# Kernel tuning notes

Measured on AMD Instinct MI355X. Metric: run time of the kernel, lower is better.

Reference implementation:

```python
import jax, jax.numpy as jnp
import numpy as np

EMBED = 1024
HEADS = 16
HEAD_DIM = EMBED // HEADS
MAX_SEQ = 5000
THETA = 10000.0
BATCH = 16
SEQ_K = 1024
SEQ_Q = 512


def _rope_tables():
    inv = 1.0 / (THETA ** (np.arange(0, EMBED, 2)[: EMBED // 2] / EMBED))
    ang = np.outer(np.arange(MAX_SEQ), inv)  # [MAX_SEQ, EMBED//2]
    return jnp.asarray(np.cos(ang), jnp.float32), jnp.asarray(np.sin(ang), jnp.float32)

COS_T, SIN_T = _rope_tables()


def _apply_rope(x, idx):
    # x: [B, S, E]; idx: [B, S]; pairs are (x[...,2i], x[...,2i+1]) across the FULL embed dim
    B, S, E = x.shape
    xp = x.reshape(B, S, E // 2, 2)
    xr, xi = xp[..., 0], xp[..., 1]
    c, s = COS_T[idx], SIN_T[idx]  # [B, S, E//2]
    return jnp.stack([xr * c - xi * s, xr * s + xi * c], axis=-1).reshape(B, S, E)


def _attn_mask(key_padding_mask):
    # (causal triu OR key padding) AND NOT eye  (eye keeps diagonal attendable), then cut query rows
    tri = jnp.triu(jnp.ones((SEQ_K, SEQ_K), bool), k=1)
    m = jnp.logical_or(tri[None], key_padding_mask[:, None, :])  # [B, K, K]
    m = jnp.logical_and(m, ~jnp.eye(SEQ_K, dtype=bool)[None])
    return m[:, -SEQ_Q:, :]  # [B, Q, K]


def setup_inputs() -> dict:
    key = jax.random.key(0)
    ks = jax.random.split(key, 16)
    def lin(i):
        W = jax.random.normal(ks[i], (EMBED, EMBED), jnp.float32) / np.sqrt(EMBED).astype(np.float32)
        b = jnp.zeros((EMBED,), jnp.float32)
        return W, b
    Wq, bq = lin(0); Wk, bk = lin(1); Wv, bv = lin(2); Wo, bo = lin(3)
    Wxr, bxr = lin(4); Wyr, byr = lin(5)
    Wxz, bxz = lin(6); Wyz, byz = lin(7)
    Wxg, bxg = lin(8); Wyg, byg = lin(9)
    key_in = jax.random.normal(ks[10], (BATCH, SEQ_K, EMBED), jnp.float32)
    key_index = jnp.sort(jax.random.randint(ks[11], (BATCH, SEQ_K), 0, MAX_SEQ), axis=-1)
    key_padding_mask = jax.random.randint(ks[12], (BATCH, SEQ_K), 0, 2).astype(bool)
    return dict(key_in=key_in, key_index=key_index, key_padding_mask=key_padding_mask,
                Wq=Wq, bq=bq, Wk=Wk, bk=bk, Wv=Wv, bv=bv, Wo=Wo, bo=bo,
                Wxr=Wxr, bxr=bxr, Wyr=Wyr, byr=byr, Wxz=Wxz, bxz=bxz,
                Wyz=Wyz, byz=byz, Wxg=Wxg, bxg=bxg, Wyg=Wyg, byg=byg)


def reference(key_in, key_index, key_padding_mask,
              Wq, bq, Wk, bk, Wv, bv, Wo, bo,
              Wxr, bxr, Wyr, byr, Wxz, bxz, Wyz, byz, Wxg, bxg, Wyg, byg):
    B = key_in.shape[0]
    # cut_query=True: query is the last SEQ_Q steps of key
    query = key_in[:, -SEQ_Q:]
    q_idx = key_index[:, -SEQ_Q:]
    q = query @ Wq + bq
    k = key_in @ Wk + bk
    v = key_in @ Wv + bv
    # RoPE applied on full embed dim BEFORE head split (as in source)
    q = _apply_rope(q, q_idx)
    k = _apply_rope(k, key_index)
    qh = q.reshape(B, SEQ_Q, HEADS, HEAD_DIM)
    kh = k.reshape(B, SEQ_K, HEADS, HEAD_DIM)
    vh = v.reshape(B, SEQ_K, HEADS, HEAD_DIM)
    mask = _attn_mask(key_padding_mask)  # [B, Q, K]
    bias = jnp.where(mask, -jnp.inf, 0.0).astype(key_in.dtype)[:, None]  # [B,1,Q,K]
    scores = jnp.einsum('bqhd,bkhd->bhqk', qh, kh) / np.float32(np.sqrt(HEAD_DIM)) + bias
    w = jax.nn.softmax(scores, axis=-1)  # [B,H,Q,K]
    o = jnp.einsum('bhqk,bkhd->bqhd', w, vh).reshape(B, SEQ_Q, EMBED)
    o = o @ Wo + bo
    # GRU-style gated residual combine (use_residual=True, use_gated=True)
    x = query
    r = jax.nn.sigmoid(x @ Wxr + bxr + o @ Wyr + byr)
    z = jax.nn.sigmoid(x @ Wxz + bxz + o @ Wyz + byz)
    h = jnp.tanh((r * x) @ Wxg + bxg + o @ Wyg + byg)
    out = (1.0 - z) * x + z * h
    attn_weights = w.mean(axis=1)  # averaged over heads, [B, Q, K]
    return out, attn_weights
```

## Files before the change

kernel.cpp:

```cpp
#include <hip/hip_runtime.h>
#include <hip/hip_bf16.h>


typedef __attribute__((ext_vector_type(8))) short bf16x8;
typedef __attribute__((ext_vector_type(4))) float f32x4;

__device__ __forceinline__ short f2bs(float f) {
  union { __hip_bfloat16 h; short s; } u; u.h = __float2bfloat16(f); return u.s;
}

static constexpr size_t OFF_WT   = 0;
static constexpr size_t OFF_TAB  = 20971520;
static constexpr size_t OFF_XBF  = 41451520;
static constexpr size_t OFF_QH   = 75005952;
static constexpr size_t OFF_KH   = 91783168;
static constexpr size_t OFF_VT   = 125337600;
static constexpr size_t OFF_KLIN = 125337600;
static constexpr size_t OFF_QLIN = 158892032;
static constexpr size_t OFF_OAT  = 158892032;
static constexpr size_t OFF_O2   = 175669248;
static constexpr size_t OFF_RB   = 75005952;
static constexpr size_t OFF_ZB   = 108560384;
static constexpr size_t OFF_RX   = 142114816;
static constexpr size_t OFF_HB   = 75005952;

__device__ __forceinline__ int swz(int q) { return ((q & 3) << 3) ^ ((q & 12) << 2); }

__global__ __launch_bounds__(256) void k_cvtx(const float* __restrict__ x,
                                              short* __restrict__ xbf) {
  size_t i = ((size_t)blockIdx.x * 256 + threadIdx.x) * 8;
  f32x4 a = *(const f32x4*)(x + i);
  f32x4 b = *(const f32x4*)(x + i + 4);
  bf16x8 o;
  o[0] = f2bs(a[0]); o[1] = f2bs(a[1]); o[2] = f2bs(a[2]); o[3] = f2bs(a[3]);
  o[4] = f2bs(b[0]); o[5] = f2bs(b[1]); o[6] = f2bs(b[2]); o[7] = f2bs(b[3]);
  *(bf16x8*)(xbf + i) = o;
}

__global__ __launch_bounds__(256) void k_table(float* __restrict__ tab) {
  int i = blockIdx.x * 256 + threadIdx.x;
  if (i >= 5000 * 512) return;
  int pos = i >> 9, fi = i & 511;
  double inv = pow(10000.0, -(double)fi / 512.0);
  double ds, dc;
  sincos((double)pos * inv, &ds, &dc);
  tab[2 * i] = (float)dc;
  tab[2 * i + 1] = (float)ds;
}

struct W10 { const float* p[10]; };
__global__ __launch_bounds__(256) void k_wt(W10 wsrc, short* __restrict__ wt) {
  __shared__ short t[32][33];
  int kb = blockIdx.x * 32, nb = blockIdx.y * 32, wi = blockIdx.z;
  const float* src = wsrc.p[wi];
  int tid = threadIdx.x;
#pragma unroll
  for (int e = 0; e < 4; ++e) {
    int idx = e * 256 + tid;
    int kr = idx >> 5, nc = idx & 31;
    t[nc][kr] = f2bs(src[(size_t)(kb + kr) * 1024 + nb + nc]);
  }
  __syncthreads();
  short* dst = wt + (size_t)wi * 1024 * 1024;
#pragma unroll
  for (int e = 0; e < 4; ++e) {
    int idx = e * 256 + tid;
    int nr = idx >> 5, kc = idx & 31;
    dst[(size_t)(nb + nr) * 1024 + kb + kc] = t[nr][kc];
  }
}

__global__ __launch_bounds__(256) void k_rope(const float* __restrict__ lin,
                                              __hip_bfloat16* __restrict__ outp,
                                              const int* __restrict__ kidx,
                                              const float* __restrict__ tab,
                                              int sh, int qoff) {
  int gid = blockIdx.x * 256 + threadIdx.x;
  int row = gid >> 9, j = gid & 511;
  int b = row >> sh, s = row & ((1 << sh) - 1);
  int idx = kidx[b * 1024 + qoff + s];
  float2 v = ((const float2*)lin)[(size_t)row * 512 + j];
  float2 cs = ((const float2*)tab)[(size_t)idx * 512 + j];
  float e0 = v.x * cs.x - v.y * cs.y;
  float e1 = v.x * cs.y + v.y * cs.x;
  int h = j >> 5, d0 = (2 * j) & 63;
  size_t o = ((size_t)(b * 16 + h) * ((size_t)1 << sh) + s) * 64 + d0;
  unsigned u = ((unsigned)(unsigned short)f2bs(e1) << 16) |
               (unsigned)(unsigned short)f2bs(e0);
  *(unsigned*)((short*)outp + o) = u;
}

enum { CM_BF16 = 0, CM_F32 = 2, CM_F32ACC = 3, CM_VT = 4 };

__global__ __launch_bounds__(256) void k_gemm(
    const short* __restrict__ A, const short* __restrict__ Bt,
    const float* __restrict__ bias, int amode, int cmode,
    void* __restrict__ Cout) {
  __shared__ __align__(16) short lA[128 * 32];
  __shared__ __align__(16) short lB[128 * 32];
  const int tid = threadIdx.x;
  const int lane = tid & 63;
  const int wv = tid >> 6;
  const int wm = wv >> 1, wn = wv & 1;
  const int lo = lane & 15, hi = lane >> 4;
  const int tm0 = blockIdx.x * 128;
  const int tn0 = blockIdx.y * 128;

  const f32x4 vz = {0.f, 0.f, 0.f, 0.f};
  f32x4 acc[4][4];
#pragma unroll
  for (int m = 0; m < 4; ++m)
#pragma unroll
    for (int n = 0; n < 4; ++n) acc[m][n] = vz;

  for (int kt = 0; kt < 32; ++kt) {
    const int k0 = kt * 32;
    __syncthreads();
#pragma unroll
    for (int i = 0; i < 2; ++i) {
      int f = i * 256 + tid;
      int r = f >> 2;
      int cb = (f & 3) * 16;
      int arow = tm0 + r;
      if (amode) arow = ((arow >> 9) << 10) + 512 + (arow & 511);
      const char* ga = (const char*)(A + (size_t)arow * 1024 + k0) + cb;
      __builtin_amdgcn_global_load_lds(
          (const __attribute__((address_space(1))) void*)ga,
          (__attribute__((address_space(3))) void*)((char*)lA + (size_t)(i * 256 + wv * 64) * 16),
          16, 0, 0);
      int brow = tn0 + r;
      const char* gb = (const char*)(Bt + (size_t)brow * 1024 + k0) + cb;
      __builtin_amdgcn_global_load_lds(
          (const __attribute__((address_space(1))) void*)gb,
          (__attribute__((address_space(3))) void*)((char*)lB + (size_t)(i * 256 + wv * 64) * 16),
          16, 0, 0);
    }
    __syncthreads();
    bf16x8 af[4], bfr[4];
#pragma unroll
    for (int m = 0; m < 4; ++m)
      af[m] = *(const bf16x8*)&lA[(wm * 64 + m * 16 + lo) * 32 + hi * 8];
#pragma unroll
    for (int n = 0; n < 4; ++n)
      bfr[n] = *(const bf16x8*)&lB[(wn * 64 + n * 16 + lo) * 32 + hi * 8];
#pragma unroll
    for (int m = 0; m < 4; ++m)
#pragma unroll
      for (int n = 0; n < 4; ++n)
        acc[m][n] = __builtin_amdgcn_mfma_f32_16x16x32_bf16(af[m], bfr[n], acc[m][n], 0, 0, 0);
  }

  if (cmode == CM_VT) {
    __hip_bfloat16* out = (__hip_bfloat16*)Cout;
#pragma unroll
    for (int m = 0; m < 4; ++m) {
      int row_base = tm0 + wm * 64 + m * 16 + hi * 4;
#pragma unroll
      for (int n = 0; n < 4; ++n) {
        int col = tn0 + wn * 64 + n * 16 + lo;
        float bsv = bias ? bias[col] : 0.f;
        int hh = col >> 6, dd = col & 63;
#pragma unroll
        for (int r = 0; r < 4; ++r) {
          int row = row_base + r;
          int bb = row >> 10, ss = row & 1023;
          out[((size_t)(bb * 16 + hh) * 64 + dd) * 1024 + ss] =
              __float2bfloat16(acc[m][n][r] + bsv);
        }
      }
    }
  } else if (cmode == CM_F32 || cmode == CM_F32ACC) {
    float* out = (float*)Cout;
#pragma unroll
    for (int m = 0; m < 4; ++m) {
      int row_base = tm0 + wm * 64 + m * 16 + hi * 4;
#pragma unroll
      for (int n = 0; n < 4; ++n) {
        int col = tn0 + wn * 64 + n * 16 + lo;
        float bsv = bias ? bias[col] : 0.f;
#pragma unroll
        for (int r = 0; r < 4; ++r) {
          size_t off = (size_t)(row_base + r) * 1024 + col;
          float val = acc[m][n][r] + bsv;
          if (cmode == CM_F32ACC) val += out[off];
          out[off] = val;
        }
      }
    }
  } else {
    __hip_bfloat16* out = (__hip_bfloat16*)Cout;
#pragma unroll
    for (int m = 0; m < 4; ++m) {
      int row_base = tm0 + wm * 64 + m * 16 + hi * 4;
#pragma unroll
      for (int n = 0; n < 4; ++n) {
        int col = tn0 + wn * 64 + n * 16 + lo;
        float bsv = bias ? bias[col] : 0.f;
#pragma unroll
        for (int r = 0; r < 4; ++r) {
          size_t off = (size_t)(row_base + r) * 1024 + col;
          out[off] = __float2bfloat16(acc[m][n][r] + bsv);
        }
      }
    }
  }
}

__global__ __launch_bounds__(512, 2) void k_attn(
    const __hip_bfloat16* __restrict__ qh,
    const __hip_bfloat16* __restrict__ kh,
    const __hip_bfloat16* __restrict__ vt,
    const unsigned char* __restrict__ padraw,
    float* __restrict__ mean_out,
    __hip_bfloat16* __restrict__ oat) {
  __shared__ float Sld[16 * 1024];
  __shared__ float osc[4 * 64 * 4];
  short* Pld = (short*)Sld;
  const int wgid = blockIdx.x;
  const int b = wgid & 15, qt = wgid >> 4;
  const int tid = threadIdx.x, lane = tid & 63, wv = tid >> 6;
  const int lo = lane & 15, hi = lane >> 4;
  const int wg = wv & 3, half = wv >> 2;
  const f32x4 vz = {0.f, 0.f, 0.f, 0.f};

  bool is_byte = false;
#pragma unroll
  for (int j = 1; j < 256; ++j)
    if ((j & 3) && padraw[j] == 1) is_byte = true;
  const int* ipad = (const int*)padraw;

  unsigned pmask = 0;
#pragma unroll
  for (int nt = 0; nt < 8; ++nt) {
    int kpos = wv * 128 + nt * 16 + lo;
    int pk = is_byte ? (int)padraw[b * 1024 + kpos]
                     : (ipad[b * 1024 + kpos] != 0 ? 1 : 0);
    pmask |= (unsigned)(pk != 0) << nt;
  }

  float macc[2][16];
#pragma unroll
  for (int rr = 0; rr < 2; ++rr)
#pragma unroll
    for (int i = 0; i < 16; ++i) macc[rr][i] = 0.f;

  const __hip_bfloat16* qbase =
      qh + ((size_t)(b * 16) * 512 + (size_t)qt * 16) * 64;
  bf16x8 qf0 = *(const bf16x8*)(qbase + (size_t)lo * 64 + hi * 8);
  bf16x8 qf1 = *(const bf16x8*)(qbase + (size_t)lo * 64 + 32 + hi * 8);

  for (int h = 0; h < 16; ++h) {
    const __hip_bfloat16* kbh = kh + (size_t)(b * 16 + h) * 1024 * 64;
    const __hip_bfloat16* vbh = vt + (size_t)(b * 16 + h) * 64 * 1024;

    bf16x8 kbuf[2][2];
#pragma unroll
    for (int p = 0; p < 2; ++p) {
      int kr = wv * 128 + p * 16 + lo;
      kbuf[p][0] = *(const bf16x8*)(kbh + (size_t)kr * 64 + hi * 8);
      kbuf[p][1] = *(const bf16x8*)(kbh + (size_t)kr * 64 + 32 + hi * 8);
    }
#pragma unroll
    for (int nt = 0; nt < 8; ++nt) {
      bf16x8 ck0 = kbuf[nt & 1][0], ck1 = kbuf[nt & 1][1];
      if (nt < 6) {
        int kr = wv * 128 + (nt + 2) * 16 + lo;
        kbuf[nt & 1][0] = *(const bf16x8*)(kbh + (size_t)kr * 64 + hi * 8);
        kbuf[nt & 1][1] = *(const bf16x8*)(kbh + (size_t)kr * 64 + 32 + hi * 8);
      }
      f32x4 sa = vz;
      sa = __builtin_amdgcn_mfma_f32_16x16x32_bf16(qf0, ck0, sa, 0, 0, 0);
      sa = __builtin_amdgcn_mfma_f32_16x16x32_bf16(qf1, ck1, sa, 0, 0, 0);
      int kpos = wv * 128 + nt * 16 + lo;
      int pk = (pmask >> nt) & 1;
#pragma unroll
      for (int r = 0; r < 4; ++r) {
        int q = hi * 4 + r;
        int qg = 512 + qt * 16 + q;
        float sv = sa[r] * 0.125f;
        bool msk = (kpos > qg) || (kpos < qg && pk != 0);
        Sld[q * 1024 + (kpos ^ swz(q))] = msk ? -1e30f : sv;
      }
    }
    __syncthreads();

#pragma unroll
    for (int rr = 0; rr < 2; ++rr) {
      int q = wv * 2 + rr;
      const int c = swz(q);
      float* row = Sld + q * 1024;
      float v[16], mx = -1e30f;
#pragma unroll
      for (int i = 0; i < 16; ++i) {
        v[i] = row[(lane + i * 64) ^ c];
        mx = fmaxf(mx, v[i]);
      }
#pragma unroll
      for (int off = 32; off > 0; off >>= 1) mx = fmaxf(mx, __shfl_xor(mx, off));
      float sum = 0.f;
#pragma unroll
      for (int i = 0; i < 16; ++i) { v[i] = __expf(v[i] - mx); sum += v[i]; }
#pragma unroll
      for (int off = 32; off > 0; off >>= 1) sum += __shfl_xor(sum, off);
      float invs = 1.0f / sum;
      short* prow = Pld + q * 2048 + 1024;
#pragma unroll
      for (int i = 0; i < 16; ++i) {
        float p = v[i] * invs;
        prow[(lane + i * 64) ^ c] = f2bs(p);
        macc[rr][i] += p;
      }
    }
    __syncthreads();

    f32x4 oacc = vz;
    {
      const short* prow = Pld + lo * 2048 + 1024;
      const int cl = swz(lo);
      const int kcg = half * 16;
      const __hip_bfloat16* vrow = vbh + (size_t)(wg * 16 + lo) * 1024;
      bf16x8 vbuf[2];
#pragma unroll
      for (int p = 0; p < 2; ++p)
        vbuf[p] = *(const bf16x8*)(vrow + (kcg + p) * 32 + hi * 8);
#pragma unroll
      for (int kc = 0; kc < 16; ++kc) {
        bf16x8 cv = vbuf[kc & 1];
        if (kc < 14)
          vbuf[kc & 1] = *(const bf16x8*)(vrow + (kcg + kc + 2) * 32 + hi * 8);
        bf16x8 pa = *(const bf16x8*)&prow[((kcg + kc) * 32 + hi * 8) ^ cl];
        oacc = __builtin_amdgcn_mfma_f32_16x16x32_bf16(pa, cv, oacc, 0, 0, 0);
      }
    }

    if (h < 15) {
      const __hip_bfloat16* qn = qbase + (size_t)(h + 1) * 512 * 64;
      qf0 = *(const bf16x8*)(qn + (size_t)lo * 64 + hi * 8);
      qf1 = *(const bf16x8*)(qn + (size_t)lo * 64 + 32 + hi * 8);
    }

    if (half == 1) {
#pragma unroll
      for (int r = 0; r < 4; ++r) osc[(wg * 64 + lane) * 4 + r] = oacc[r];
    }
    __syncthreads();
    if (half == 0) {
#pragma unroll
      for (int r = 0; r < 4; ++r) {
        float o = oacc[r] + osc[(wg * 64 + lane) * 4 + r];
        int q = qt * 16 + hi * 4 + r;
        oat[((size_t)b * 512 + q) * 1024 + h * 64 + wg * 16 + lo] =
            __float2bfloat16(o);
      }
    }
  }

#pragma unroll
  for (int rr = 0; rr < 2; ++rr) {
    size_t mrow = ((size_t)b * 512 + (size_t)qt * 16 + wv * 2 + rr) * 1024;
#pragma unroll
    for (int i = 0; i < 16; ++i)
      mean_out[mrow + lane + i * 64] = macc[rr][i] * 0.0625f;
  }
}

__global__ __launch_bounds__(256) void k_rx(const float* __restrict__ Rb,
                                            const float* __restrict__ x,
                                            short* __restrict__ rx) {
  size_t base = ((size_t)blockIdx.x * 256 + threadIdx.x) * 4;
  int row = (int)(base >> 10), col = (int)(base & 1023);
  int b = row >> 9, s = row & 511;
  const float* xp = x + ((size_t)(b * 1024 + 512 + s) << 10) + col;
  f32x4 rv = *(const f32x4*)(Rb + base);
  f32x4 xv = *(const f32x4*)xp;
  typedef __attribute__((ext_vector_type(4))) short s16x4;
  s16x4 o;
#pragma unroll
  for (int j = 0; j < 4; ++j) {
    float r = 1.f / (1.f + __expf(-rv[j]));
    o[j] = f2bs(r * xv[j]);
  }
  *(s16x4*)(rx + base) = o;
}

__global__ __launch_bounds__(256) void k_final(const float* __restrict__ Zb,
                                               const float* __restrict__ Hb,
                                               const float* __restrict__ x,
                                               float* __restrict__ out0) {
  size_t base = ((size_t)blockIdx.x * 256 + threadIdx.x) * 4;
  int row = (int)(base >> 10), col = (int)(base & 1023);
  int b = row >> 9, s = row & 511;
  const float* xp = x + ((size_t)(b * 1024 + 512 + s) << 10) + col;
  f32x4 zv = *(const f32x4*)(Zb + base);
  f32x4 hv = *(const f32x4*)(Hb + base);
  f32x4 xv = *(const f32x4*)xp;
  f32x4 o;
#pragma unroll
  for (int j = 0; j < 4; ++j) {
    float z = 1.f / (1.f + __expf(-zv[j]));
    float hh = tanhf(hv[j]);
    o[j] = (1.f - z) * xv[j] + z * hh;
  }
  *(f32x4*)(out0 + base) = o;
}

extern "C" void kernel_launch(void* const* d_in, const int* in_sizes, int n_in,
                              void* d_out, int out_size, void* d_ws, size_t ws_size,
                              hipStream_t stream) {
  const float* key_in = (const float*)d_in[0];
  const int* key_index = (const int*)d_in[1];
  const unsigned char* pad = (const unsigned char*)d_in[2];
  const float* W[10] = {(const float*)d_in[3],  (const float*)d_in[5],
                        (const float*)d_in[7],  (const float*)d_in[9],
                        (const float*)d_in[11], (const float*)d_in[13],
                        (const float*)d_in[15], (const float*)d_in[17],
                        (const float*)d_in[19], (const float*)d_in[21]};
  const float* bq  = (const float*)d_in[4];
  const float* bk  = (const float*)d_in[6];
  const float* bv  = (const float*)d_in[8];
  const float* bo  = (const float*)d_in[10];
  const float* bxr = (const float*)d_in[12];
  const float* byr = (const float*)d_in[14];
  const float* bxz = (const float*)d_in[16];
  const float* byz = (const float*)d_in[18];
  const float* bxg = (const float*)d_in[20];
  const float* byg = (const float*)d_in[22];

  char* ws = (char*)d_ws;
  short* wt = (short*)(ws + OFF_WT);
  float* tab = (float*)(ws + OFF_TAB);
  short* xbf = (short*)(ws + OFF_XBF);
  __hip_bfloat16* qh = (__hip_bfloat16*)(ws + OFF_QH);
  __hip_bfloat16* kh = (__hip_bfloat16*)(ws + OFF_KH);
  __hip_bfloat16* vt = (__hip_bfloat16*)(ws + OFF_VT);
  float* qlin = (float*)(ws + OFF_QLIN);
  float* klin = (float*)(ws + OFF_KLIN);
  float* Rb = (float*)(ws + OFF_RB);
  float* Zb = (float*)(ws + OFF_ZB);
  __hip_bfloat16* oat = (__hip_bfloat16*)(ws + OFF_OAT);
  short* o2 = (short*)(ws + OFF_O2);
  short* rx = (short*)(ws + OFF_RX);
  float* Hb = (float*)(ws + OFF_HB);

  float* out0 = (float*)d_out;
  float* out1 = out0 + (size_t)8388608;

  W10 wargs;
  for (int i = 0; i < 10; ++i) wargs.p[i] = W[i];
  k_cvtx<<<8192, 256, 0, stream>>>(key_in, xbf);
  k_wt<<<dim3(32, 32, 10), 256, 0, stream>>>(wargs, wt);
  k_table<<<10000, 256, 0, stream>>>(tab);

  k_gemm<<<dim3(64, 8), 256, 0, stream>>>(xbf, wt + (size_t)0 * 1048576, bq, 1, CM_F32,
                                          (void*)qlin);
  k_rope<<<16384, 256, 0, stream>>>(qlin, qh, key_index, tab, 9, 512);
  k_gemm<<<dim3(128, 8), 256, 0, stream>>>(xbf, wt + (size_t)1 * 1048576, bk, 0, CM_F32,
                                           (void*)klin);
  k_rope<<<32768, 256, 0, stream>>>(klin, kh, key_index, tab, 10, 0);
  k_gemm<<<dim3(128, 8), 256, 0, stream>>>(xbf, wt + (size_t)2 * 1048576, bv, 0, CM_VT,
                                           (void*)vt);

  k_attn<<<dim3(512), 512, 0, stream>>>(qh, kh, vt, pad, out1, oat);

  k_gemm<<<dim3(64, 8), 256, 0, stream>>>((const short*)oat, wt + (size_t)3 * 1048576, bo,
                                          0, CM_BF16, (void*)o2);
  k_gemm<<<dim3(64, 8), 256, 0, stream>>>(xbf, wt + (size_t)4 * 1048576, bxr, 1, CM_F32,
                                          (void*)Rb);
  k_gemm<<<dim3(64, 8), 256, 0, stream>>>(o2, wt + (size_t)5 * 1048576, byr, 0, CM_F32ACC,
                                          (void*)Rb);
  k_gemm<<<dim3(64, 8), 256, 0, stream>>>(xbf, wt + (size_t)6 * 1048576, bxz, 1, CM_F32,
                                          (void*)Zb);
  k_gemm<<<dim3(64, 8), 256, 0, stream>>>(o2, wt + (size_t)7 * 1048576, byz, 0, CM_F32ACC,
                                          (void*)Zb);
  k_rx<<<8192, 256, 0, stream>>>(Rb, key_in, rx);
  k_gemm<<<dim3(64, 8), 256, 0, stream>>>(rx, wt + (size_t)8 * 1048576, bxg, 0, CM_F32,
                                          (void*)Hb);
  k_gemm<<<dim3(64, 8), 256, 0, stream>>>(o2, wt + (size_t)9 * 1048576, byg, 0, CM_F32ACC,
                                          (void*)Hb);
  k_final<<<8192, 256, 0, stream>>>(Zb, Hb, key_in, out0);
}
```

Measured before the change: 837.4 us.

## Fuse RoPE into Q/K GEMM epilogue and merge gate GEMM pairs

Applies RoPE directly in the Q and K projection GEMM epilogues, using a lane shuffle to fetch the paired element. This removes the fp32 qlin/klin round trips and the two separate rope kernels. The r and z gate weights are reordered so each pair of gate GEMMs runs as one wider GEMM writing an interleaved RbZb buffer with ldc 2048, halving those launches. It also precomputes inverse frequencies once for the table kernel and reuses attention's shared memory as the reduction scratch, at the cost of an extra barrier and per-element table/index gathers in the GEMM epilogue.

New measurement: 1.025 ms. +22.5%, slower.

```diff
diff --git a/kernel.cpp b/kernel.cpp
--- a/kernel.cpp
+++ b/kernel.cpp
@@ -15,14 +15,12 @@
 static constexpr size_t OFF_QH   = 75005952;
 static constexpr size_t OFF_KH   = 91783168;
 static constexpr size_t OFF_VT   = 125337600;
-static constexpr size_t OFF_KLIN = 125337600;
-static constexpr size_t OFF_QLIN = 158892032;
 static constexpr size_t OFF_OAT  = 158892032;
 static constexpr size_t OFF_O2   = 175669248;
-static constexpr size_t OFF_RB   = 75005952;
-static constexpr size_t OFF_ZB   = 108560384;
+static constexpr size_t OFF_INV  = OFF_OAT;
+static constexpr size_t OFF_RBZB = 75005952;
 static constexpr size_t OFF_RX   = 142114816;
-static constexpr size_t OFF_HB   = 75005952;
+static constexpr size_t OFF_HB   = OFF_XBF;
 
 __device__ __forceinline__ int swz(int q) { return ((q & 3) << 3) ^ ((q & 12) << 2); }
 
@@ -37,13 +35,17 @@
   *(bf16x8*)(xbf + i) = o;
 }
 
-__global__ __launch_bounds__(256) void k_table(float* __restrict__ tab) {
+__global__ void k_tabinv(double* __restrict__ inv) {
+  int i = threadIdx.x;
+  inv[i] = pow(10000.0, -(double)i / 512.0);
+}
+__global__ __launch_bounds__(256) void k_table(float* __restrict__ tab,
+                                               const double* __restrict__ inv) {
   int i = blockIdx.x * 256 + threadIdx.x;
   if (i >= 5000 * 512) return;
   int pos = i >> 9, fi = i & 511;
-  double inv = pow(10000.0, -(double)fi / 512.0);
   double ds, dc;
-  sincos((double)pos * inv, &ds, &dc);
+  sincos((double)pos * inv[fi], &ds, &dc);
   tab[2 * i] = (float)dc;
   tab[2 * i + 1] = (float)ds;
 }
@@ -70,32 +72,14 @@
   }
 }
 
-__global__ __launch_bounds__(256) void k_rope(const float* __restrict__ lin,
-                                              __hip_bfloat16* __restrict__ outp,
-                                              const int* __restrict__ kidx,
-                                              const float* __restrict__ tab,
-                                              int sh, int qoff) {
-  int gid = blockIdx.x * 256 + threadIdx.x;
-  int row = gid >> 9, j = gid & 511;
-  int b = row >> sh, s = row & ((1 << sh) - 1);
-  int idx = kidx[b * 1024 + qoff + s];
-  float2 v = ((const float2*)lin)[(size_t)row * 512 + j];
-  float2 cs = ((const float2*)tab)[(size_t)idx * 512 + j];
-  float e0 = v.x * cs.x - v.y * cs.y;
-  float e1 = v.x * cs.y + v.y * cs.x;
-  int h = j >> 5, d0 = (2 * j) & 63;
-  size_t o = ((size_t)(b * 16 + h) * ((size_t)1 << sh) + s) * 64 + d0;
-  unsigned u = ((unsigned)(unsigned short)f2bs(e1) << 16) |
-               (unsigned)(unsigned short)f2bs(e0);
-  *(unsigned*)((short*)outp + o) = u;
-}
-
-enum { CM_BF16 = 0, CM_F32 = 2, CM_F32ACC = 3, CM_VT = 4 };
+enum { CM_BF16 = 0, CM_F32 = 2, CM_F32ACC = 3, CM_VT = 4, CM_ROPE = 5 };
 
 __global__ __launch_bounds__(256) void k_gemm(
     const short* __restrict__ A, const short* __restrict__ Bt,
-    const float* __restrict__ bias, int amode, int cmode,
-    void* __restrict__ Cout) {
+    const float* __restrict__ bias, const float* __restrict__ bias2,
+    int amode, int cmode, void* __restrict__ Cout, int ldc,
+    const float* __restrict__ tab, const int* __restrict__ kidx,
+    int sshift, int qoff) {
   __shared__ __align__(16) short lA[128 * 32];
   __shared__ __align__(16) short lB[128 * 32];
   const int tid = threadIdx.x;
@@ -150,7 +134,33 @@
         acc[m][n] = __builtin_amdgcn_mfma_f32_16x16x32_bf16(af[m], bfr[n], acc[m][n], 0, 0, 0);
   }
 
-  if (cmode == CM_VT) {
+  if (cmode == CM_ROPE) {
+    __hip_bfloat16* out = (__hip_bfloat16*)Cout;
+    const float2* t2 = (const float2*)tab;
+    const int srows = 1 << sshift;
+    const float sgn = (lane & 1) ? 1.f : -1.f;
+#pragma unroll
+    for (int m = 0; m < 4; ++m) {
+      int row_base = tm0 + wm * 64 + m * 16 + hi * 4;
+#pragma unroll
+      for (int n = 0; n < 4; ++n) {
+        int col = tn0 + wn * 64 + n * 16 + lo;
+        float bsv = bias[col];
+        int j = col >> 1, hh = col >> 6, dd = col & 63;
+#pragma unroll
+        for (int r = 0; r < 4; ++r) {
+          int row = row_base + r;
+          int bb = row >> sshift, ss = row & (srows - 1);
+          int idx = kidx[bb * 1024 + qoff + ss];
+          float2 cs = t2[(size_t)idx * 512 + j];
+          float val = acc[m][n][r] + bsv;
+          float part = __shfl_xor(val, 1);
+          float rot = val * cs.x + sgn * part * cs.y;
+          out[((size_t)(bb * 16 + hh) * srows + ss) * 64 + dd] = __float2bfloat16(rot);
+        }
+      }
+    }
+  } else if (cmode == CM_VT) {
     __hip_bfloat16* out = (__hip_bfloat16*)Cout;
 #pragma unroll
     for (int m = 0; m < 4; ++m) {
@@ -177,10 +187,10 @@
 #pragma unroll
       for (int n = 0; n < 4; ++n) {
         int col = tn0 + wn * 64 + n * 16 + lo;
-        float bsv = bias ? bias[col] : 0.f;
+        float bsv = bias ? ((col < 1024 || !bias2) ? bias[col] : bias2[col - 1024]) : 0.f;
 #pragma unroll
         for (int r = 0; r < 4; ++r) {
-          size_t off = (size_t)(row_base + r) * 1024 + col;
+          size_t off = (size_t)(row_base + r) * ldc + col;
           float val = acc[m][n][r] + bsv;
           if (cmode == CM_F32ACC) val += out[off];
           out[off] = val;
@@ -198,7 +208,7 @@
         float bsv = bias ? bias[col] : 0.f;
 #pragma unroll
         for (int r = 0; r < 4; ++r) {
-          size_t off = (size_t)(row_base + r) * 1024 + col;
+          size_t off = (size_t)(row_base + r) * ldc + col;
           out[off] = __float2bfloat16(acc[m][n][r] + bsv);
         }
       }
@@ -214,7 +224,6 @@
     float* __restrict__ mean_out,
     __hip_bfloat16* __restrict__ oat) {
   __shared__ float Sld[16 * 1024];
-  __shared__ float osc[4 * 64 * 4];
   short* Pld = (short*)Sld;
   const int wgid = blockIdx.x;
   const int b = wgid & 15, qt = wgid >> 4;
@@ -223,6 +232,8 @@
   const int wg = wv & 3, half = wv >> 2;
   const f32x4 vz = {0.f, 0.f, 0.f, 0.f};
 
+  auto oscw = [&](int idx) -> float& { return Sld[(idx >> 9) * 1024 + (idx & 511)]; };
+
   bool is_byte = false;
 #pragma unroll
   for (int j = 1; j < 256; ++j)
@@ -341,18 +352,19 @@
 
     if (half == 1) {
 #pragma unroll
-      for (int r = 0; r < 4; ++r) osc[(wg * 64 + lane) * 4 + r] = oacc[r];
+      for (int r = 0; r < 4; ++r) oscw((wg * 64 + lane) * 4 + r) = oacc[r];
     }
     __syncthreads();
     if (half == 0) {
 #pragma unroll
       for (int r = 0; r < 4; ++r) {
-        float o = oacc[r] + osc[(wg * 64 + lane) * 4 + r];
+        float o = oacc[r] + oscw((wg * 64 + lane) * 4 + r);
         int q = qt * 16 + hi * 4 + r;
         oat[((size_t)b * 512 + q) * 1024 + h * 64 + wg * 16 + lo] =
             __float2bfloat16(o);
       }
     }
+    __syncthreads();
   }
 
 #pragma unroll
@@ -364,14 +376,14 @@
   }
 }
 
-__global__ __launch_bounds__(256) void k_rx(const float* __restrict__ Rb,
+__global__ __launch_bounds__(256) void k_rx(const float* __restrict__ RbZb,
                                             const float* __restrict__ x,
                                             short* __restrict__ rx) {
   size_t base = ((size_t)blockIdx.x * 256 + threadIdx.x) * 4;
   int row = (int)(base >> 10), col = (int)(base & 1023);
   int b = row >> 9, s = row & 511;
   const float* xp = x + ((size_t)(b * 1024 + 512 + s) << 10) + col;
-  f32x4 rv = *(const f32x4*)(Rb + base);
+  f32x4 rv = *(const f32x4*)(RbZb + (size_t)row * 2048 + col);
   f32x4 xv = *(const f32x4*)xp;
   typedef __attribute__((ext_vector_type(4))) short s16x4;
   s16x4 o;
@@ -383,7 +395,7 @@
   *(s16x4*)(rx + base) = o;
 }
 
-__global__ __launch_bounds__(256) void k_final(const float* __restrict__ Zb,
+__global__ __launch_bounds__(256) void k_final(const float* __restrict__ RbZb,
                                                const float* __restrict__ Hb,
                                                const float* __restrict__ x,
                                                float* __restrict__ out0) {
@@ -391,7 +403,7 @@
   int row = (int)(base >> 10), col = (int)(base & 1023);
   int b = row >> 9, s = row & 511;
   const float* xp = x + ((size_t)(b * 1024 + 512 + s) << 10) + col;
-  f32x4 zv = *(const f32x4*)(Zb + base);
+  f32x4 zv = *(const f32x4*)(RbZb + (size_t)row * 2048 + 1024 + col);
   f32x4 hv = *(const f32x4*)(Hb + base);
   f32x4 xv = *(const f32x4*)xp;
   f32x4 o;
@@ -410,11 +422,6 @@
   const float* key_in = (const float*)d_in[0];
   const int* key_index = (const int*)d_in[1];
   const unsigned char* pad = (const unsigned char*)d_in[2];
-  const float* W[10] = {(const float*)d_in[3],  (const float*)d_in[5],
-                        (const float*)d_in[7],  (const float*)d_in[9],
-                        (const float*)d_in[11], (const float*)d_in[13],
-                        (const float*)d_in[15], (const float*)d_in[17],
-                        (const float*)d_in[19], (const float*)d_in[21]};
   const float* bq  = (const float*)d_in[4];
   const float* bk  = (const float*)d_in[6];
   const float* bv  = (const float*)d_in[8];
@@ -433,10 +440,8 @@
   __hip_bfloat16* qh = (__hip_bfloat16*)(ws + OFF_QH);
   __hip_bfloat16* kh = (__hip_bfloat16*)(ws + OFF_KH);
   __hip_bfloat16* vt = (__hip_bfloat16*)(ws + OFF_VT);
-  float* qlin = (float*)(ws + OFF_QLIN);
-  float* klin = (float*)(ws + OFF_KLIN);
-  float* Rb = (float*)(ws + OFF_RB);
-  float* Zb = (float*)(ws + OFF_ZB);
+  double* inv = (double*)(ws + OFF_INV);
+  float* RbZb = (float*)(ws + OFF_RBZB);
   __hip_bfloat16* oat = (__hip_bfloat16*)(ws + OFF_OAT);
   short* o2 = (short*)(ws + OFF_O2);
   short* rx = (short*)(ws + OFF_RX);
@@ -446,36 +451,46 @@
   float* out1 = out0 + (size_t)8388608;
 
   W10 wargs;
-  for (int i = 0; i < 10; ++i) wargs.p[i] = W[i];
+  wargs.p[0] = (const float*)d_in[3];
+  wargs.p[1] = (const float*)d_in[5];
+  wargs.p[2] = (const float*)d_in[7];
+  wargs.p[3] = (const float*)d_in[9];
+  wargs.p[4] = (const float*)d_in[11];
+  wargs.p[5] = (const float*)d_in[15];
+  wargs.p[6] = (const float*)d_in[13];
+  wargs.p[7] = (const float*)d_in[17];
+  wargs.p[8] = (const float*)d_in[19];
+  wargs.p[9] = (const float*)d_in[21];
+
   k_cvtx<<<8192, 256, 0, stream>>>(key_in, xbf);
   k_wt<<<dim3(32, 32, 10), 256, 0, stream>>>(wargs, wt);
-  k_table<<<10000, 256, 0, stream>>>(tab);
-
-  k_gemm<<<dim3(64, 8), 256, 0, stream>>>(xbf, wt + (size_t)0 * 1048576, bq, 1, CM_F32,
-                                          (void*)qlin);
-  k_rope<<<16384, 256, 0, stream>>>(qlin, qh, key_index, tab, 9, 512);
-  k_gemm<<<dim3(128, 8), 256, 0, stream>>>(xbf, wt + (size_t)1 * 1048576, bk, 0, CM_F32,
-                                           (void*)klin);
-  k_rope<<<32768, 256, 0, stream>>>(klin, kh, key_index, tab, 10, 0);
-  k_gemm<<<dim3(128, 8), 256, 0, stream>>>(xbf, wt + (size_t)2 * 1048576, bv, 0, CM_VT,
-                                           (void*)vt);
+  k_tabinv<<<1, 512, 0, stream>>>(inv);
+  k_table<<<10000, 256, 0, stream>>>(tab, inv);
+
+  k_gemm<<<dim3(64, 8), 256, 0, stream>>>(xbf, wt + (size_t)0 * 1048576, bq, nullptr,
+                                          1, CM_ROPE, (void*)qh, 0, tab, key_index, 9, 512);
+  k_gemm<<<dim3(128, 8), 256, 0, stream>>>(xbf, wt + (size_t)1 * 1048576, bk, nullptr,
+                                           0, CM_ROPE, (void*)kh, 0, tab, key_index, 10, 0);
+  k_gemm<<<dim3(128, 8), 256, 0, stream>>>(xbf, wt + (size_t)2 * 1048576, bv, nullptr,
+                                           0, CM_VT, (void*)vt, 0, nullptr, nullptr, 0, 0);
 
   k_attn<<<dim3(512), 512, 0, stream>>>(qh, kh, vt, pad, out1, oat);
 
   k_gemm<<<dim3(64, 8), 256, 0, stream>>>((const short*)oat, wt + (size_t)3 * 1048576, bo,
-                                          0, CM_BF16, (void*)o2);
-  k_gemm<<<dim3(64, 8), 256, 0, stream>>>(xbf, wt + (size_t)4 * 1048576, bxr, 1, CM_F32,
-                                          (void*)Rb);
-  k_gemm<<<dim3(64, 8), 256, 0, stream>>>(o2, wt + (size_t)5 * 1048576, byr, 0, CM_F32ACC,
-                                          (void*)Rb);
-  k_gemm<<<dim3(64, 8), 256, 0, stream>>>(xbf, wt + (size_t)6 * 1048576, bxz, 1, CM_F32,
-                                          (void*)Zb);
-  k_gemm<<<dim3(64, 8), 256, 0, stream>>>(o2, wt + (size_t)7 * 1048576, byz, 0, CM_F32ACC,
-                                          (void*)Zb);
-  k_rx<<<8192, 256, 0, stream>>>(Rb, key_in, rx);
-  k_gemm<<<dim3(64, 8), 256, 0, stream>>>(rx, wt + (size_t)8 * 1048576, bxg, 0, CM_F32,
-                                          (void*)Hb);
-  k_gemm<<<dim3(64, 8), 256, 0, stream>>>(o2, wt + (size_t)9 * 1048576, byg, 0, CM_F32ACC,
-                                          (void*)Hb);
-  k_final<<<8192, 256, 0, stream>>>(Zb, Hb, key_in, out0);
-}
+                                          nullptr, 0, CM_BF16, (void*)o2, 1024,
+                                          nullptr, nullptr, 0, 0);
+  k_gemm<<<dim3(64, 16), 256, 0, stream>>>(xbf, wt + (size_t)4 * 1048576, bxr, bxz,
+                                           1, CM_F32, (void*)RbZb, 2048,
+                                           nullptr, nullptr, 0, 0);
+  k_gemm<<<dim3(64, 16), 256, 0, stream>>>(o2, wt + (size_t)6 * 1048576, byr, byz,
+                                           0, CM_F32ACC, (void*)RbZb, 2048,
+                                           nullptr, nullptr, 0, 0);
+  k_rx<<<8192, 256, 0, stream>>>(RbZb, key_in, rx);
+  k_gemm<<<dim3(64, 8), 256, 0, stream>>>(rx, wt + (size_t)8 * 1048576, bxg, nullptr,
+                                          0, CM_F32, (void*)Hb, 1024,
+                                          nullptr, nullptr, 0, 0);
+  k_gemm<<<dim3(64, 8), 256, 0, stream>>>(o2, wt + (size_t)9 * 1048576, byg, nullptr,
+                                          0, CM_F32ACC, (void*)Hb, 1024,
+                                          nullptr, nullptr, 0, 0);
+  k_final<<<8192, 256, 0, stream>>>(RbZb, Hb, key_in, out0);
+}
```
